# Performance work log

Hardware: AMD Instinct MI355X
Metric: run time of the kernel (lower is better)

Reference implementation:

```python
import jax, jax.numpy as jnp
import numpy as np

N = 50000      # nodes
E = 800000     # edges per metapath
M = 3          # metapaths
H = 2          # heads
IN = 128       # in_dim
HID = 64       # hidden
HEAD = HID // H
OUT = 16       # classes
ATT = 128      # atten_dim


def setup_inputs() -> dict:
    key = jax.random.key(0)
    ks = jax.random.split(key, 12)
    s = 0.05
    return {
        "x": jax.random.normal(ks[0], (N, IN), jnp.float32),
        "edge_index": jax.random.randint(ks[1], (M, 2, E), 0, N, dtype=jnp.int64),
        # per-(metapath, head) GCN params
        "W_enc": jax.random.normal(ks[2], (M, H, IN, HID), jnp.float32) * s,
        "b_enc": jnp.zeros((M, H, HID), jnp.float32),
        "W_conv": jax.random.normal(ks[3], (M, H, HID, HID), jnp.float32) * s,
        "b_conv": jnp.zeros((M, H, HID), jnp.float32),
        "W_dec": jax.random.normal(ks[4], (M, H, HID, HEAD), jnp.float32) * s,
        "b_dec": jnp.zeros((M, H, HEAD), jnp.float32),
        # semantic attention params
        "W_s": jax.random.normal(ks[5], (HID, ATT), jnp.float32) * s,
        "b_s": jnp.zeros((ATT,), jnp.float32),
        "q": jax.random.normal(ks[6], (ATT,), jnp.float32) * s,
        # output projection
        "W_o": jax.random.normal(ks[7], (HID, OUT), jnp.float32) * s,
        "b_o": jnp.zeros((OUT,), jnp.float32),
    }


def _lrelu(v, slope=0.1):
    return jnp.where(v > 0, v, slope * v)


def reference(x, edge_index, W_enc, b_enc, W_conv, b_conv, W_dec, b_dec, W_s, b_s, q, W_o, b_o):
    # encoder for all (metapath, head) at once: [M,H,N,HID]
    h = _lrelu(jnp.einsum('ni,mhio->mhno', x, W_enc) + b_enc[:, :, None, :])

    z_list = []
    for m in range(M):  # small fixed number of metapaths
        src = edge_index[m, 0]
        dst = edge_index[m, 1]
        # GCNConv with self-loops + symmetric normalization (PyG semantics)
        deg = jax.ops.segment_sum(jnp.ones(E, jnp.float32), dst, num_segments=N) + 1.0
        inv_sqrt = jax.lax.rsqrt(deg)
        coef = inv_sqrt[src] * inv_sqrt[dst]                 # [E]
        xw = jnp.einsum('hnd,hdo->hno', h[m], W_conv[m])     # [H,N,HID]
        msg = xw[:, src, :] * coef[None, :, None]            # [H,E,HID] gather
        agg = jax.vmap(lambda mm: jax.ops.segment_sum(mm, dst, num_segments=N))(msg)
        agg = agg + xw * (1.0 / deg)[None, :, None]          # self-loop term (norm = 1/deg)
        agg = agg + b_conv[m][:, None, :]
        hh = _lrelu(agg)
        dec = jnp.einsum('hnd,hdo->hno', hh, W_dec[m]) + b_dec[m][:, None, :]  # [H,N,HEAD]
        z_list.append(jnp.transpose(dec, (1, 0, 2)).reshape(N, HID))           # head concat

    zs = jnp.stack(z_list)                                   # [M,N,HID]
    # semantic attention over metapaths
    hs = jnp.tanh(jnp.einsum('mnd,da->mna', zs, W_s) + b_s)
    beta = jax.nn.softmax(jnp.einsum('mna,a->mn', hs, q).mean(axis=1))  # [M]
    Z = jnp.einsum('m,mnd->nd', beta, zs)                    # [N,HID]
    out = jax.nn.log_softmax(Z @ W_o + b_o, axis=-1)         # [N,OUT]
    return out, beta
```

## Files before the change

### kernel.cpp

```cpp
#include <hip/hip_runtime.h>

#define NN 50000
#define EE 800000
#define MM 3
#define HH 2
#define IND 128
#define HIDD 64
#define HEADD 32
#define OUTD 16
#define ATTD 128

#define NBKT 64
#define BSZ 782

#define NG4 200000
#define BBLK 196
#define QCAP 13200

#define GLS 136
#define XWN 50048

typedef unsigned char u8;
typedef unsigned short u16;
typedef unsigned long long u64;
typedef short bf16x8 __attribute__((ext_vector_type(8)));
typedef unsigned short u16x8 __attribute__((ext_vector_type(8)));
typedef u64 u64x2 __attribute__((ext_vector_type(2)));
typedef unsigned int u32x4 __attribute__((ext_vector_type(4)));
typedef float f32x2 __attribute__((ext_vector_type(2)));
typedef float f32x4 __attribute__((ext_vector_type(4)));

__device__ __forceinline__ float lrelu(float v) { return v > 0.f ? v : 0.1f * v; }

__device__ __forceinline__ float fast_tanh(float x) {
    float ax = fabsf(x);
    float e = __expf(-2.0f * ax);
    float t = (1.0f - e) * __builtin_amdgcn_rcpf(1.0f + e);
    return copysignf(t, x);
}

__device__ __forceinline__ u16 f2b(float f) {
    union { float f; unsigned int u; } v; v.f = f;
    unsigned int r = v.u + 0x7fffu + ((v.u >> 16) & 1u);
    return (u16)(r >> 16);
}
__device__ __forceinline__ float b2f(u16 u) {
    union { unsigned int u; float f; } v; v.u = ((unsigned int)u) << 16; return v.f;
}

__device__ __forceinline__ u8 f2e4hw(float f) {
    int r = __builtin_amdgcn_cvt_pk_fp8_f32(f, f, 0, false);
    return (u8)(r & 0xff);
}

__device__ __forceinline__ void acc16(f32x2* acc, u32x4 w) {
#pragma unroll
    for (int i = 0; i < 4; i++) {
        acc[2 * i]     += __builtin_amdgcn_cvt_pk_f32_fp8(w[i], false);
        acc[2 * i + 1] += __builtin_amdgcn_cvt_pk_f32_fp8(w[i], true);
    }
}

__global__ __launch_bounds__(256) void k_bucket(const int* __restrict__ ei,
                                                u64* __restrict__ queues,
                                                int* __restrict__ gcur) {
    __shared__ int cnt[NBKT];
    __shared__ int base[NBKT];
    const int m = blockIdx.y, tid = threadIdx.x;
    const int4* s4 = (const int4*)(ei + (size_t)m * 2 * EE);
    const int4* d4 = (const int4*)(ei + (size_t)m * 2 * EE + EE);
    const int q0 = blockIdx.x * 1024;
    if (tid < NBKT) cnt[tid] = 0;
    __syncthreads();
#pragma unroll
    for (int i = 0; i < 4; i++) {
        int q = q0 + i * 256 + tid;
        if (q < NG4) {
            int4 v = d4[q];
            atomicAdd(&cnt[v.x / BSZ], 1);
            atomicAdd(&cnt[v.y / BSZ], 1);
            atomicAdd(&cnt[v.z / BSZ], 1);
            atomicAdd(&cnt[v.w / BSZ], 1);
        }
    }
    __syncthreads();
    if (tid < NBKT) { base[tid] = atomicAdd(&gcur[m * NBKT + tid], cnt[tid]); cnt[tid] = 0; }
    __syncthreads();
#pragma unroll
    for (int i = 0; i < 4; i++) {
        int q = q0 + i * 256 + tid;
        if (q < NG4) {
            int4 dv = d4[q];
            int4 sv = s4[q];
            int ds[4] = {dv.x, dv.y, dv.z, dv.w};
            int ss[4] = {sv.x, sv.y, sv.z, sv.w};
#pragma unroll
            for (int e = 0; e < 4; e++) {
                int b = ds[e] / BSZ;
                int slot = base[b] + atomicAdd(&cnt[b], 1);
                if (slot < QCAP) {
                    u64 pk = ((u64)(unsigned)ds[e] << 32) | (unsigned)ss[e];
                    queues[((size_t)(m * NBKT + b)) * QCAP + slot] = pk;
                }
            }
        }
    }
}

__global__ void k_pscan(const int* __restrict__ gcur, int* __restrict__ pbase) {
    int t = threadIdx.x;
    if (t < MM) {
        int run = 0;
        for (int b = 0; b < NBKT; b++) {
            int L = gcur[t * NBKT + b]; if (L > QCAP) L = QCAP;
            pbase[t * NBKT + b] = run; run += L;
        }
    }
}

__global__ __launch_bounds__(512) void k_csr(const u64* __restrict__ queues,
                                             const int* __restrict__ gcur,
                                             const int* __restrict__ pbase,
                                             int* __restrict__ ofs,
                                             float* __restrict__ rs,
                                             int* __restrict__ sorted) {
    __shared__ int cnt[BSZ];
    __shared__ int wscan[8];
    const int m = blockIdx.y;
    const int b = blockIdx.x;
    const int tid = threadIdx.x;
    const int lane = tid & 63, w = tid >> 6;
    int qlen = gcur[m * NBKT + b]; if (qlen > QCAP) qlen = QCAP;
    const u64* q = queues + ((size_t)(m * NBKT + b)) * QCAP;
    const u64x2* q2 = (const u64x2*)q;
    const int dlo = b * BSZ;
    const int nd = min(dlo + BSZ, NN) - dlo;
    const int n2 = qlen >> 1;
    for (int i = tid; i < BSZ; i += 512) cnt[i] = 0;
    __syncthreads();
    for (int i = tid; i < n2; i += 512) {
        u64x2 e = q2[i];
        atomicAdd(&cnt[(int)(e.x >> 32) - dlo], 1);
        atomicAdd(&cnt[(int)(e.y >> 32) - dlo], 1);
    }
    if (tid == 0 && (qlen & 1))
        atomicAdd(&cnt[(int)(q[qlen - 1] >> 32) - dlo], 1);
    __syncthreads();
    const int c0 = tid * 2;
    int v0 = (c0 < BSZ) ? cnt[c0] : 0;
    int v1 = (c0 + 1 < BSZ) ? cnt[c0 + 1] : 0;
    int s = v0 + v1;
    int vv = s;
    for (int off = 1; off < 64; off <<= 1) { int t = __shfl_up(vv, off); if (lane >= off) vv += t; }
    if (lane == 63) wscan[w] = vv;
    __syncthreads();
    if (tid == 0) { int run = 0; for (int j = 0; j < 8; j++) { int t = wscan[j]; wscan[j] = run; run += t; } }
    __syncthreads();
    int excl = wscan[w] + vv - s;
    int g0 = pbase[m * NBKT + b] + excl;
    int g1 = g0 + v0;
    if (c0 < nd) {
        ofs[(size_t)m * (NN + 1) + dlo + c0] = g0;
        rs[(size_t)m * NN + dlo + c0] = rsqrtf((float)(v0 + 1));
    }
    if (c0 + 1 < nd) {
        ofs[(size_t)m * (NN + 1) + dlo + c0 + 1] = g1;
        rs[(size_t)m * NN + dlo + c0 + 1] = rsqrtf((float)(v1 + 1));
    }
    if (b == NBKT - 1 && tid == 0)
        ofs[(size_t)m * (NN + 1) + NN] = EE;
    __syncthreads();
    if (c0 < BSZ) cnt[c0] = g0;
    if (c0 + 1 < BSZ) cnt[c0 + 1] = g1;
    __syncthreads();
    int* srt = sorted + (size_t)m * EE;
    for (int i = tid; i < n2; i += 512) {
        u64x2 e = q2[i];
        int p0 = atomicAdd(&cnt[(int)(e.x >> 32) - dlo], 1);
        srt[p0] = (int)(e.x & 0xffffffffu);
        int p1 = atomicAdd(&cnt[(int)(e.y >> 32) - dlo], 1);
        srt[p1] = (int)(e.y & 0xffffffffu);
    }
    if (tid == 0 && (qlen & 1)) {
        u64 e = q[qlen - 1];
        int p0 = atomicAdd(&cnt[(int)(e >> 32) - dlo], 1);
        srt[p0] = (int)(e & 0xffffffffu);
    }
}

__global__ __launch_bounds__(256) void k_prep(const float* __restrict__ We, const float* __restrict__ Wc,
                                              const float* __restrict__ Wd, const float* __restrict__ Ws,
                                              u16* __restrict__ wbe, u16* __restrict__ wbc,
                                              u16* __restrict__ wbd, u16* __restrict__ wbs) {
    int t = blockIdx.x * 256 + threadIdx.x;
    if (t >= 11776) return;
    bf16x8 val;
    u16* dst;
    if (t < 6144) {
        int m = t >> 11, r = t & 2047;
        int nt = r >> 8, ks = (r >> 6) & 3, lane = r & 63;
        int n = nt * 16 + (lane & 15), h = n >> 6, o = n & 63;
        int kb = ks * 32 + (lane >> 4) * 8;
        const float* w = We + ((size_t)(m * 2 + h) * 128) * 64;
#pragma unroll
        for (int j = 0; j < 8; j++) val[j] = (short)f2b(w[(size_t)(kb + j) * 64 + o]);
        dst = wbe + ((size_t)m * 2048 + r) * 8;
    } else if (t < 9216) {
        int u = t - 6144;
        int m = u >> 10, r = u & 1023;
        int nt = r >> 7, ks = (r >> 6) & 1, lane = r & 63;
        int h = nt >> 2, o = (nt & 3) * 16 + (lane & 15);
        int kb = ks * 32 + (lane >> 4) * 8;
        const float* w = Wc + ((size_t)(m * 2 + h) * 64) * 64;
#pragma unroll
        for (int j = 0; j < 8; j++) val[j] = (short)f2b(w[(size_t)(kb + j) * 64 + o]);
        dst = wbc + ((size_t)m * 1024 + r) * 8;
    } else if (t < 10752) {
        int u = t - 9216;
        int m = u >> 9, r = u & 511;
        int nt = r >> 7, ks = (r >> 6) & 1, lane = r & 63;
        int h = nt >> 1, o = (nt & 1) * 16 + (lane & 15);
        int kb = ks * 32 + (lane >> 4) * 8;
        const float* w = Wd + ((size_t)(m * 2 + h) * 64) * 32;
#pragma unroll
        for (int j = 0; j < 8; j++) val[j] = (short)f2b(w[(size_t)(kb + j) * 32 + o]);
        dst = wbd + ((size_t)m * 512 + r) * 8;
    } else {
        int r = t - 10752;
        int nt = r >> 7, ks = (r >> 6) & 1, lane = r & 63;
        int n = nt * 16 + (lane & 15);
        int kb = ks * 32 + (lane >> 4) * 8;
#pragma unroll
        for (int j = 0; j < 8; j++) val[j] = (short)f2b(Ws[(size_t)(kb + j) * 128 + n]);
        dst = wbs + (size_t)r * 8;
    }
    *(bf16x8*)dst = val;
}

#define HLS 133
__global__ __launch_bounds__(256) void k_encconv(const float* __restrict__ x,
                                                 const u16* __restrict__ wbe_all,
                                                 const float* __restrict__ be_all,
                                                 const u16* __restrict__ wbc_all,
                                                 const float* __restrict__ rs_all,
                                                 u8* __restrict__ xw_all) {
    __shared__ float hl[64 * HLS];
    const int m = blockIdx.y;
    const int tid = threadIdx.x, lane = tid & 63, wave = tid >> 6;
    const int quad = lane >> 4, c16 = lane & 15;
    const int row = blockIdx.x * 64 + wave * 16 + c16;
    const bool ok = row < NN;
    const bf16x8* wbE = (const bf16x8*)(wbe_all + (size_t)m * 2048 * 8);
    const float* be = be_all + m * 2 * 64;
    const float* rs = rs_all + (size_t)m * NN;
    u8* xw = xw_all + (size_t)m * XWN * 128;
    f32x4 zero = {0.f, 0.f, 0.f, 0.f};
    f32x4 acc[8];
#pragma unroll
    for (int nt = 0; nt < 8; nt++) acc[nt] = zero;
#pragma unroll
    for (int ks = 0; ks < 4; ks++) {
        bf16x8 a = {0, 0, 0, 0, 0, 0, 0, 0};
        if (ok) {
            const float* xp = x + (size_t)row * 128 + ks * 32 + quad * 8;
            float4 xa = *(const float4*)xp;
            float4 xb = *(const float4*)(xp + 4);
            a[0] = (short)f2b(xa.x); a[1] = (short)f2b(xa.y);
            a[2] = (short)f2b(xa.z); a[3] = (short)f2b(xa.w);
            a[4] = (short)f2b(xb.x); a[5] = (short)f2b(xb.y);
            a[6] = (short)f2b(xb.z); a[7] = (short)f2b(xb.w);
        }
#pragma unroll
        for (int nt = 0; nt < 8; nt++)
            acc[nt] = __builtin_amdgcn_mfma_f32_16x16x32_bf16(a, wbE[(nt * 4 + ks) * 64 + lane], acc[nt], 0, 0, 0);
    }
    const int rbl = wave * 16 + quad * 4;
#pragma unroll
    for (int nt = 0; nt < 8; nt++) {
        int col = nt * 16 + c16, hh = col >> 6, o = col & 63;
        float bias = be[hh * 64 + o];
#pragma unroll
        for (int j = 0; j < 4; j++) {
            int rl = rbl + j;
            int rg = blockIdx.x * 64 + rl;
            hl[rl * HLS + col] = (rg < NN) ? lrelu(acc[nt][j] + bias) : 0.f;
        }
    }
    __syncthreads();
    const bf16x8* wbC = (const bf16x8*)(wbc_all + (size_t)m * 1024 * 8);
    f32x4 cacc[8];
#pragma unroll
    for (int nt = 0; nt < 8; nt++) cacc[nt] = zero;
    const int rl = wave * 16 + c16;
#pragma unroll
    for (int ks = 0; ks < 2; ks++) {
        bf16x8 a0, a1;
        const float* hp = &hl[rl * HLS + ks * 32 + quad * 8];
#pragma unroll
        for (int j = 0; j < 8; j++) { a0[j] = (short)f2b(hp[j]); a1[j] = (short)f2b(hp[64 + j]); }
#pragma unroll
        for (int nt = 0; nt < 8; nt++)
            cacc[nt] = __builtin_amdgcn_mfma_f32_16x16x32_bf16(nt < 4 ? a0 : a1, wbC[(nt * 2 + ks) * 64 + lane], cacc[nt], 0, 0, 0);
    }
    float rsv[4];
#pragma unroll
    for (int j = 0; j < 4; j++) {
        int r = blockIdx.x * 64 + rbl + j;
        rsv[j] = (r < NN) ? rs[r] * 64.f : 0.f;
    }
#pragma unroll
    for (int nt = 0; nt < 8; nt++) {
        int col = nt * 16 + c16;
#pragma unroll
        for (int j = 0; j < 4; j++) {
            int r = blockIdx.x * 64 + rbl + j;
            xw[(size_t)r * 128 + col] = f2e4hw(cacc[nt][j] * rsv[j]);
        }
    }
}

__global__ __launch_bounds__(512) void k_gpost(const int* __restrict__ sorted_all,
                                               const int* __restrict__ ofs_all,
                                               const float* __restrict__ rs_all,
                                               const u8* __restrict__ xw_all,
                                               const float* __restrict__ bconv_all,
                                               const u16* __restrict__ wbd_all,
                                               const float* __restrict__ bdec_all,
                                               const u16* __restrict__ wbs,
                                               const float* __restrict__ bs,
                                               const float* __restrict__ qv,
                                               u16* __restrict__ z_all,
                                               float* __restrict__ score) {
    __shared__ u16 shm[64 * GLS];
    __shared__ float spart[8];
    u16* ggl = shm;
    float* zl = (float*)shm;
    const int m = blockIdx.y;
    const int tid = threadIdx.x, lane = tid & 63, wave = tid >> 6;
    const int* sorted = sorted_all + (size_t)m * EE;
    const int* ofs = ofs_all + (size_t)m * (NN + 1);
    const float* rs = rs_all + (size_t)m * NN;
    const u8* xw = xw_all + (size_t)m * XWN * 128;
    const float* bconv = bconv_all + m * 2 * 64;
    const float* bdec = bdec_all + m * 2 * 32;
    u16* z = z_all + (size_t)m * NN * 64;

    {
        const int g = lane >> 3, c = lane & 7;
        const int wbase = blockIdx.x * 64 + wave * 8;
        const int dst = wbase + g;
        int ov = 0;
        { int ii = wbase + lane; if (lane < 9) ov = ofs[ii > NN ? NN : ii]; }
        const int beg = __shfl(ov, g);
        const int deg = __shfl(ov, g + 1) - beg;
        int degmax = max(deg, __shfl_xor(deg, 8));
        degmax = max(degmax, __shfl_xor(degmax, 16));
        degmax = max(degmax, __shfl_xor(degmax, 32));
        const int coff = c * 16;

        auto lidx = [&](int j) -> int {
            int t = j + (c & 3);
            return (t < deg) ? sorted[beg + t] : NN;
        };
        auto lrow = [&](int iv, u32x4* wv) {
#pragma unroll
            for (int k = 0; k < 4; k++) {
                int s = __shfl(iv, (lane & 0x38) + k);
                wv[k] = *(const u32x4*)&xw[(size_t)(unsigned)s * 128 + coff];
            }
        };

        f32x2 acc[8];
#pragma unroll
        for (int i = 0; i < 8; i++) acc[i] = 0.f;

        int i0 = lidx(0);
        int i1 = lidx(4);
        {
            int sd = dst < NN ? dst : NN;
            u32x4 w = *(const u32x4*)&xw[(size_t)sd * 128 + coff];
            acc16(acc, w);
        }
        u32x4 wA[4], wB[4];
        lrow(i0, wA);
        const int nch = ((degmax + 7) >> 3) * 2;
        for (int ch = 0; ch < nch; ch += 2) {
            lrow(i1, wB);
            i0 = lidx(ch * 4 + 8);
#pragma unroll
            for (int k = 0; k < 4; k++) acc16(acc, wA[k]);
            lrow(i0, wA);
            i1 = lidx(ch * 4 + 12);
#pragma unroll
            for (int k = 0; k < 4; k++) acc16(acc, wB[k]);
        }

        float rsv = (dst < NN) ? rs[dst] * (1.f / 64.f) : 0.f;
        u16x8 o0, o1;
#pragma unroll
        for (int i = 0; i < 4; i++) {
            o0[2 * i]     = f2b(acc[i].x * rsv);
            o0[2 * i + 1] = f2b(acc[i].y * rsv);
            o1[2 * i]     = f2b(acc[i + 4].x * rsv);
            o1[2 * i + 1] = f2b(acc[i + 4].y * rsv);
        }
        u16* gp = &ggl[(wave * 8 + g) * GLS + coff];
        *(u16x8*)gp = o0;
        *(u16x8*)(gp + 8) = o1;
    }
    __syncthreads();

    f32x4 zero = {0.f, 0.f, 0.f, 0.f};
    const int quad = lane >> 4, c16 = lane & 15;
    const int wq = wave & 3, hi = wave >> 2;
    const int rl = wq * 16 + c16;
    const bf16x8* wd = (const bf16x8*)(wbd_all + (size_t)m * 512 * 8);
    f32x4 pacc[2];
    pacc[0] = zero; pacc[1] = zero;
#pragma unroll
    for (int ks = 0; ks < 2; ks++) {
        bf16x8 a;
        int k0 = ks * 32 + quad * 8;
        const u16* gp = &ggl[rl * GLS + hi * 64 + k0];
#pragma unroll
        for (int j = 0; j < 8; j++)
            a[j] = (short)f2b(lrelu(b2f(gp[j]) + bconv[hi * 64 + k0 + j]));
#pragma unroll
        for (int nt2 = 0; nt2 < 2; nt2++) {
            int nt = hi * 2 + nt2;
            pacc[nt2] = __builtin_amdgcn_mfma_f32_16x16x32_bf16(a, wd[(nt * 2 + ks) * 64 + lane], pacc[nt2], 0, 0, 0);
        }
    }
    __syncthreads();
    {
        const int rbl = wq * 16 + quad * 4;
#pragma unroll
        for (int nt2 = 0; nt2 < 2; nt2++) {
            int nt = hi * 2 + nt2;
            int col = nt * 16 + c16, hh = col >> 5, o = col & 31;
            float bias = bdec[hh * 32 + o];
#pragma unroll
            for (int j = 0; j < 4; j++) {
                int rl2 = rbl + j;
                int rg = blockIdx.x * 64 + rl2;
                zl[rl2 * 68 + col] = (rg < NN) ? (pacc[nt2][j] + bias) : 0.f;
            }
        }
    }
    __syncthreads();

    {
        int rl2 = tid >> 3, cq = tid & 7;
        int rg = blockIdx.x * 64 + rl2;
        if (rg < NN) {
#pragma unroll
            for (int i = 0; i < 2; i++) {
                int c4 = (cq * 2 + i) * 4;
                float4 zv = *(const float4*)&zl[rl2 * 68 + c4];
                ushort4 o;
                o.x = f2b(zv.x); o.y = f2b(zv.y); o.z = f2b(zv.z); o.w = f2b(zv.w);
                *(ushort4*)&z[(size_t)rg * 64 + c4] = o;
            }
        }
    }
    float s = 0.f;
    {
        const bf16x8* wsb = (const bf16x8*)wbs;
        f32x4 sa[4];
#pragma unroll
        for (int nt2 = 0; nt2 < 4; nt2++) sa[nt2] = zero;
#pragma unroll
        for (int ks = 0; ks < 2; ks++) {
            bf16x8 a;
            const float* zp = &zl[rl * 68 + ks * 32 + quad * 8];
#pragma unroll
            for (int j = 0; j < 8; j++) a[j] = (short)f2b(zp[j]);
#pragma unroll
            for (int nt2 = 0; nt2 < 4; nt2++) {
                int nt = hi * 4 + nt2;
                sa[nt2] = __builtin_amdgcn_mfma_f32_16x16x32_bf16(a, wsb[(nt * 2 + ks) * 64 + lane], sa[nt2], 0, 0, 0);
            }
        }
        const int rbl = wq * 16 + quad * 4;
#pragma unroll
        for (int nt2 = 0; nt2 < 4; nt2++) {
            int nt = hi * 4 + nt2;
            int col = nt * 16 + c16;
            float qc = qv[col], bb = bs[col];
#pragma unroll
            for (int j = 0; j < 4; j++) {
                int rg = blockIdx.x * 64 + rbl + j;
                if (rg < NN) s += fast_tanh(sa[nt2][j] + bb) * qc;
            }
        }
#pragma unroll
        for (int off = 1; off < 64; off <<= 1) s += __shfl_xor(s, off);
    }
    if (lane == 0) spart[wave] = s;
    __syncthreads();
    if (tid == 0) {
        float t = spart[0] + spart[1] + spart[2] + spart[3]
                + spart[4] + spart[5] + spart[6] + spart[7];
        atomicAdd(&score[m], t);
    }
}

__global__ void k_beta(const float* __restrict__ score, float* __restrict__ beta_ws,
                       float* __restrict__ out) {
    if (threadIdx.x == 0) {
        float s0 = score[0] / (float)NN, s1 = score[1] / (float)NN, s2 = score[2] / (float)NN;
        float mx = fmaxf(s0, fmaxf(s1, s2));
        float e0 = expf(s0 - mx), e1 = expf(s1 - mx), e2 = expf(s2 - mx);
        float inv = 1.f / (e0 + e1 + e2);
        beta_ws[0] = e0 * inv; beta_ws[1] = e1 * inv; beta_ws[2] = e2 * inv;
        out[800000] = e0 * inv; out[800001] = e1 * inv; out[800002] = e2 * inv;
    }
}

__global__ __launch_bounds__(256) void k_out(const u16* __restrict__ z,
                                             const float* __restrict__ beta,
                                             const float* __restrict__ Wo,
                                             const float* __restrict__ bo,
                                             float* __restrict__ out) {
    __shared__ float Zt[64 * 68];
    __shared__ float Wl[64 * 16];
    __shared__ float bl[16];
    const int tid = threadIdx.x, nbase = blockIdx.x * 64;
    float b0 = beta[0], b1 = beta[1], b2 = beta[2];
    for (int qq = tid; qq < 64 * 16; qq += 256) {
        int node = qq >> 4, k4 = qq & 15;
        int ng = nbase + node;
        float4 v = make_float4(0.f, 0.f, 0.f, 0.f);
        if (ng < NN) {
            ushort4 z0 = *(const ushort4*)&z[((size_t)0 * NN + ng) * 64 + k4 * 4];
            ushort4 z1 = *(const ushort4*)&z[((size_t)1 * NN + ng) * 64 + k4 * 4];
            ushort4 z2 = *(const ushort4*)&z[((size_t)2 * NN + ng) * 64 + k4 * 4];
            v.x = b0 * b2f(z0.x) + b1 * b2f(z1.x) + b2 * b2f(z2.x);
            v.y = b0 * b2f(z0.y) + b1 * b2f(z1.y) + b2 * b2f(z2.y);
            v.z = b0 * b2f(z0.z) + b1 * b2f(z1.z) + b2 * b2f(z2.z);
            v.w = b0 * b2f(z0.w) + b1 * b2f(z1.w) + b2 * b2f(z2.w);
        }
        *(float4*)&Zt[node * 68 + k4 * 4] = v;
    }
    for (int qq = tid; qq < 64 * 16 / 4; qq += 256)
        ((float4*)Wl)[qq] = ((const float4*)Wo)[qq];
    if (tid < 16) bl[tid] = bo[tid];
    __syncthreads();

    const int node = tid >> 2, cg = tid & 3;
    float4 a = make_float4(bl[cg * 4 + 0], bl[cg * 4 + 1], bl[cg * 4 + 2], bl[cg * 4 + 3]);
    for (int k = 0; k < 64; k++) {
        float zv = Zt[node * 68 + k];
        float4 w = *(const float4*)&Wl[k * 16 + cg * 4];
        a.x = fmaf(zv, w.x, a.x);
        a.y = fmaf(zv, w.y, a.y);
        a.z = fmaf(zv, w.z, a.z);
        a.w = fmaf(zv, w.w, a.w);
    }
    float mx = fmaxf(fmaxf(a.x, a.y), fmaxf(a.z, a.w));
    mx = fmaxf(mx, __shfl_xor(mx, 1));
    mx = fmaxf(mx, __shfl_xor(mx, 2));
    float sm = expf(a.x - mx) + expf(a.y - mx) + expf(a.z - mx) + expf(a.w - mx);
    sm += __shfl_xor(sm, 1);
    sm += __shfl_xor(sm, 2);
    float lse = mx + logf(sm);
    int ng = nbase + node;
    if (ng < NN) {
        float4 r = make_float4(a.x - lse, a.y - lse, a.z - lse, a.w - lse);
        *(float4*)&out[(size_t)ng * 16 + cg * 4] = r;
    }
}

extern "C" void kernel_launch(void* const* d_in, const int* in_sizes, int n_in,
                              void* d_out, int out_size, void* d_ws, size_t ws_size,
                              hipStream_t stream) {
    const float* x      = (const float*)d_in[0];
    const int*   ei     = (const int*)d_in[1];
    const float* W_enc  = (const float*)d_in[2];
    const float* b_enc  = (const float*)d_in[3];
    const float* W_conv = (const float*)d_in[4];
    const float* b_conv = (const float*)d_in[5];
    const float* W_dec  = (const float*)d_in[6];
    const float* b_dec  = (const float*)d_in[7];
    const float* W_s    = (const float*)d_in[8];
    const float* b_s    = (const float*)d_in[9];
    const float* qv     = (const float*)d_in[10];
    const float* W_o    = (const float*)d_in[11];
    const float* b_o    = (const float*)d_in[12];
    float* out = (float*)d_out;

    char* ws = (char*)d_ws;
    size_t off = 0;
    auto alloc = [&](size_t bytes) -> char* {
        char* p = ws + off;
        off = (off + bytes + 255) & ~(size_t)255;
        return p;
    };
    int*   row_ofs = (int*)alloc((size_t)MM * (NN + 1) * 4);
    float* rs      = (float*)alloc((size_t)MM * NN * 4);
    int*   sorted  = (int*)alloc((size_t)MM * EE * 4);
    u64*   queues  = (u64*)alloc((size_t)MM * NBKT * QCAP * 8);
    int*   gcur    = (int*)alloc((size_t)MM * NBKT * 4);
    int*   pbase   = (int*)alloc((size_t)MM * NBKT * 4);
    float* score   = (float*)alloc(64);
    float* beta_ws = (float*)alloc(64);
    u16*   wbe     = (u16*)alloc((size_t)MM * 2048 * 8 * 2);
    u16*   wbc     = (u16*)alloc((size_t)MM * 1024 * 8 * 2);
    u16*   wbd     = (u16*)alloc((size_t)MM * 512 * 8 * 2);
    u16*   wbs     = (u16*)alloc((size_t)1024 * 8 * 2);
    u8*    xw_buf  = (u8*)alloc((size_t)MM * XWN * 128);
    u16*   z_buf   = (u16*)alloc((size_t)MM * NN * 64 * 2);

    hipMemsetAsync(gcur, 0, (size_t)MM * NBKT * 4, stream);
    hipMemsetAsync(score, 0, 16, stream);

    dim3 gbkt(BBLK, MM);
    dim3 gcsr(NBKT, MM);
    k_bucket<<<gbkt, 256, 0, stream>>>(ei, queues, gcur);
    k_pscan<<<1, 64, 0, stream>>>(gcur, pbase);
    k_csr<<<gcsr, 512, 0, stream>>>(queues, gcur, pbase, row_ofs, rs, sorted);
    k_prep<<<46, 256, 0, stream>>>(W_enc, W_conv, W_dec, W_s, wbe, wbc, wbd, wbs);

    const int GB = (NN + 63) / 64;
    dim3 gmm(GB, MM);
    k_encconv<<<gmm, 256, 0, stream>>>(x, wbe, b_enc, wbc, rs, xw_buf);
    k_gpost<<<gmm, 512, 0, stream>>>(sorted, row_ofs, rs, xw_buf,
                                     b_conv, wbd, b_dec, wbs, b_s, qv,
                                     z_buf, score);
    k_beta<<<1, 64, 0, stream>>>(score, beta_ws, out);
    k_out<<<GB, 256, 0, stream>>>(z_buf, beta_ws, W_o, b_o, out);
}
```

Before: 248.1 us.

## Sort gather rows by degree per block and reuse x across metapaths in encoder

Adds a small kernel that ranks each 64-node group by in-degree, so that the gather kernel assigns nodes with similar degree to the same 8-lane group within a wave. This reduces divergence from the per-wave max-degree loop. The encoder kernel now loads and converts each x row once and loops over all three metapaths, instead of launching one block per metapath and rereading x each time. It also vectorizes a few LDS reads. The cost is an extra launch plus a perm buffer, and fewer but longer encoder blocks.

```diff
diff --git a/kernel.cpp b/kernel.cpp
--- a/kernel.cpp
+++ b/kernel.cpp
@@ -19,6 +19,7 @@
 
 #define GLS 136
 #define XWN 50048
+#define PN  50048
 
 typedef unsigned char u8;
 typedef unsigned short u16;
@@ -188,6 +189,29 @@
     }
 }
 
+__global__ __launch_bounds__(256) void k_perm(const int* __restrict__ ofs_all,
+                                              int* __restrict__ perm_all) {
+    __shared__ int dl[256];
+    const int m = blockIdx.y;
+    const int t = threadIdx.x;
+    const int sub = t >> 6, li = t & 63;
+    const int base = blockIdx.x * 256 + sub * 64;
+    const int* ofs = ofs_all + (size_t)m * (NN + 1);
+    const int g = base + li;
+    int d = (g < NN) ? (ofs[g + 1] - ofs[g]) : -1;
+    dl[t] = d;
+    __syncthreads();
+    if (base < PN) {
+        const int* dls = &dl[sub * 64];
+        int rank = 0;
+        for (int j = 0; j < 64; j++) {
+            int dj = dls[j];
+            rank += (dj > d || (dj == d && j < li)) ? 1 : 0;
+        }
+        perm_all[(size_t)m * PN + base + rank] = li;
+    }
+}
+
 __global__ __launch_bounds__(256) void k_prep(const float* __restrict__ We, const float* __restrict__ Wc,
                                               const float* __restrict__ Wd, const float* __restrict__ Ws,
                                               u16* __restrict__ wbe, u16* __restrict__ wbc,
@@ -245,82 +269,93 @@
                                                  const float* __restrict__ rs_all,
                                                  u8* __restrict__ xw_all) {
     __shared__ float hl[64 * HLS];
-    const int m = blockIdx.y;
     const int tid = threadIdx.x, lane = tid & 63, wave = tid >> 6;
     const int quad = lane >> 4, c16 = lane & 15;
     const int row = blockIdx.x * 64 + wave * 16 + c16;
     const bool ok = row < NN;
-    const bf16x8* wbE = (const bf16x8*)(wbe_all + (size_t)m * 2048 * 8);
-    const float* be = be_all + m * 2 * 64;
-    const float* rs = rs_all + (size_t)m * NN;
-    u8* xw = xw_all + (size_t)m * XWN * 128;
+    const int rbl = wave * 16 + quad * 4;
+    const int rl = wave * 16 + c16;
     f32x4 zero = {0.f, 0.f, 0.f, 0.f};
-    f32x4 acc[8];
-#pragma unroll
-    for (int nt = 0; nt < 8; nt++) acc[nt] = zero;
+
+    bf16x8 a[4];
 #pragma unroll
     for (int ks = 0; ks < 4; ks++) {
-        bf16x8 a = {0, 0, 0, 0, 0, 0, 0, 0};
+        bf16x8 t = {0, 0, 0, 0, 0, 0, 0, 0};
         if (ok) {
             const float* xp = x + (size_t)row * 128 + ks * 32 + quad * 8;
             float4 xa = *(const float4*)xp;
             float4 xb = *(const float4*)(xp + 4);
-            a[0] = (short)f2b(xa.x); a[1] = (short)f2b(xa.y);
-            a[2] = (short)f2b(xa.z); a[3] = (short)f2b(xa.w);
-            a[4] = (short)f2b(xb.x); a[5] = (short)f2b(xb.y);
-            a[6] = (short)f2b(xb.z); a[7] = (short)f2b(xb.w);
-        }
-#pragma unroll
-        for (int nt = 0; nt < 8; nt++)
-            acc[nt] = __builtin_amdgcn_mfma_f32_16x16x32_bf16(a, wbE[(nt * 4 + ks) * 64 + lane], acc[nt], 0, 0, 0);
-    }
-    const int rbl = wave * 16 + quad * 4;
-#pragma unroll
-    for (int nt = 0; nt < 8; nt++) {
-        int col = nt * 16 + c16, hh = col >> 6, o = col & 63;
-        float bias = be[hh * 64 + o];
-#pragma unroll
-        for (int j = 0; j < 4; j++) {
-            int rl = rbl + j;
-            int rg = blockIdx.x * 64 + rl;
-            hl[rl * HLS + col] = (rg < NN) ? lrelu(acc[nt][j] + bias) : 0.f;
-        }
-    }
-    __syncthreads();
-    const bf16x8* wbC = (const bf16x8*)(wbc_all + (size_t)m * 1024 * 8);
-    f32x4 cacc[8];
-#pragma unroll
-    for (int nt = 0; nt < 8; nt++) cacc[nt] = zero;
-    const int rl = wave * 16 + c16;
-#pragma unroll
-    for (int ks = 0; ks < 2; ks++) {
-        bf16x8 a0, a1;
-        const float* hp = &hl[rl * HLS + ks * 32 + quad * 8];
-#pragma unroll
-        for (int j = 0; j < 8; j++) { a0[j] = (short)f2b(hp[j]); a1[j] = (short)f2b(hp[64 + j]); }
-#pragma unroll
-        for (int nt = 0; nt < 8; nt++)
-            cacc[nt] = __builtin_amdgcn_mfma_f32_16x16x32_bf16(nt < 4 ? a0 : a1, wbC[(nt * 2 + ks) * 64 + lane], cacc[nt], 0, 0, 0);
-    }
-    float rsv[4];
-#pragma unroll
-    for (int j = 0; j < 4; j++) {
-        int r = blockIdx.x * 64 + rbl + j;
-        rsv[j] = (r < NN) ? rs[r] * 64.f : 0.f;
-    }
-#pragma unroll
-    for (int nt = 0; nt < 8; nt++) {
-        int col = nt * 16 + c16;
+            t[0] = (short)f2b(xa.x); t[1] = (short)f2b(xa.y);
+            t[2] = (short)f2b(xa.z); t[3] = (short)f2b(xa.w);
+            t[4] = (short)f2b(xb.x); t[5] = (short)f2b(xb.y);
+            t[6] = (short)f2b(xb.z); t[7] = (short)f2b(xb.w);
+        }
+        a[ks] = t;
+    }
+
+    for (int m = 0; m < MM; m++) {
+        const bf16x8* wbE = (const bf16x8*)(wbe_all + (size_t)m * 2048 * 8);
+        const float* be = be_all + m * 2 * 64;
+        const float* rs = rs_all + (size_t)m * NN;
+        u8* xw = xw_all + (size_t)m * XWN * 128;
+
+        f32x4 acc[8];
+#pragma unroll
+        for (int nt = 0; nt < 8; nt++) acc[nt] = zero;
+#pragma unroll
+        for (int ks = 0; ks < 4; ks++) {
+#pragma unroll
+            for (int nt = 0; nt < 8; nt++)
+                acc[nt] = __builtin_amdgcn_mfma_f32_16x16x32_bf16(a[ks], wbE[(nt * 4 + ks) * 64 + lane], acc[nt], 0, 0, 0);
+        }
+#pragma unroll
+        for (int nt = 0; nt < 8; nt++) {
+            int col = nt * 16 + c16, hh = col >> 6, o = col & 63;
+            float bias = be[hh * 64 + o];
+#pragma unroll
+            for (int j = 0; j < 4; j++) {
+                int rlw = rbl + j;
+                int rg = blockIdx.x * 64 + rlw;
+                hl[rlw * HLS + col] = (rg < NN) ? lrelu(acc[nt][j] + bias) : 0.f;
+            }
+        }
+        __syncthreads();
+        const bf16x8* wbC = (const bf16x8*)(wbc_all + (size_t)m * 1024 * 8);
+        f32x4 cacc[8];
+#pragma unroll
+        for (int nt = 0; nt < 8; nt++) cacc[nt] = zero;
+#pragma unroll
+        for (int ks = 0; ks < 2; ks++) {
+            bf16x8 a0, a1;
+            const float* hp = &hl[rl * HLS + ks * 32 + quad * 8];
+#pragma unroll
+            for (int j = 0; j < 8; j++) { a0[j] = (short)f2b(hp[j]); a1[j] = (short)f2b(hp[64 + j]); }
+#pragma unroll
+            for (int nt = 0; nt < 8; nt++)
+                cacc[nt] = __builtin_amdgcn_mfma_f32_16x16x32_bf16(nt < 4 ? a0 : a1, wbC[(nt * 2 + ks) * 64 + lane], cacc[nt], 0, 0, 0);
+        }
+        float rsv[4];
 #pragma unroll
         for (int j = 0; j < 4; j++) {
             int r = blockIdx.x * 64 + rbl + j;
-            xw[(size_t)r * 128 + col] = f2e4hw(cacc[nt][j] * rsv[j]);
-        }
+            rsv[j] = (r < NN) ? rs[r] * 64.f : 0.f;
+        }
+#pragma unroll
+        for (int nt = 0; nt < 8; nt++) {
+            int col = nt * 16 + c16;
+#pragma unroll
+            for (int j = 0; j < 4; j++) {
+                int r = blockIdx.x * 64 + rbl + j;
+                xw[(size_t)r * 128 + col] = f2e4hw(cacc[nt][j] * rsv[j]);
+            }
+        }
+        if (m < MM - 1) __syncthreads();
     }
 }
 
 __global__ __launch_bounds__(512) void k_gpost(const int* __restrict__ sorted_all,
                                                const int* __restrict__ ofs_all,
+                                               const int* __restrict__ perm_all,
                                                const float* __restrict__ rs_all,
                                                const u8* __restrict__ xw_all,
                                                const float* __restrict__ bconv_all,
@@ -339,6 +374,7 @@
     const int tid = threadIdx.x, lane = tid & 63, wave = tid >> 6;
     const int* sorted = sorted_all + (size_t)m * EE;
     const int* ofs = ofs_all + (size_t)m * (NN + 1);
+    const int* perm = perm_all + (size_t)m * PN;
     const float* rs = rs_all + (size_t)m * NN;
     const u8* xw = xw_all + (size_t)m * XWN * 128;
     const float* bconv = bconv_all + m * 2 * 64;
@@ -347,12 +383,11 @@
 
     {
         const int g = lane >> 3, c = lane & 7;
-        const int wbase = blockIdx.x * 64 + wave * 8;
-        const int dst = wbase + g;
-        int ov = 0;
-        { int ii = wbase + lane; if (lane < 9) ov = ofs[ii > NN ? NN : ii]; }
-        const int beg = __shfl(ov, g);
-        const int deg = __shfl(ov, g + 1) - beg;
+        const int pl = perm[blockIdx.x * 64 + wave * 8 + g];
+        const int dst = blockIdx.x * 64 + pl;
+        const bool on = dst < NN;
+        int beg = 0, deg = 0;
+        if (on) { beg = ofs[dst]; deg = ofs[dst + 1] - beg; }
         int degmax = max(deg, __shfl_xor(deg, 8));
         degmax = max(degmax, __shfl_xor(degmax, 16));
         degmax = max(degmax, __shfl_xor(degmax, 32));
@@ -377,7 +412,7 @@
         int i0 = lidx(0);
         int i1 = lidx(4);
         {
-            int sd = dst < NN ? dst : NN;
+            int sd = on ? dst : NN;
             u32x4 w = *(const u32x4*)&xw[(size_t)sd * 128 + coff];
             acc16(acc, w);
         }
@@ -395,7 +430,7 @@
             for (int k = 0; k < 4; k++) acc16(acc, wB[k]);
         }
 
-        float rsv = (dst < NN) ? rs[dst] * (1.f / 64.f) : 0.f;
+        float rsv = on ? rs[dst] * (1.f / 64.f) : 0.f;
         u16x8 o0, o1;
 #pragma unroll
         for (int i = 0; i < 4; i++) {
@@ -404,7 +439,7 @@
             o1[2 * i]     = f2b(acc[i + 4].x * rsv);
             o1[2 * i + 1] = f2b(acc[i + 4].y * rsv);
         }
-        u16* gp = &ggl[(wave * 8 + g) * GLS + coff];
+        u16* gp = &ggl[pl * GLS + coff];
         *(u16x8*)gp = o0;
         *(u16x8*)(gp + 8) = o1;
     }
@@ -421,10 +456,10 @@
     for (int ks = 0; ks < 2; ks++) {
         bf16x8 a;
         int k0 = ks * 32 + quad * 8;
-        const u16* gp = &ggl[rl * GLS + hi * 64 + k0];
+        u16x8 gv = *(const u16x8*)&ggl[rl * GLS + hi * 64 + k0];
 #pragma unroll
         for (int j = 0; j < 8; j++)
-            a[j] = (short)f2b(lrelu(b2f(gp[j]) + bconv[hi * 64 + k0 + j]));
+            a[j] = (short)f2b(lrelu(b2f(gv[j]) + bconv[hi * 64 + k0 + j]));
 #pragma unroll
         for (int nt2 = 0; nt2 < 2; nt2++) {
             int nt = hi * 2 + nt2;
@@ -473,8 +508,12 @@
         for (int ks = 0; ks < 2; ks++) {
             bf16x8 a;
             const float* zp = &zl[rl * 68 + ks * 32 + quad * 8];
-#pragma unroll
-            for (int j = 0; j < 8; j++) a[j] = (short)f2b(zp[j]);
+            f32x4 z0 = *(const f32x4*)zp;
+            f32x4 z1 = *(const f32x4*)(zp + 4);
+            a[0] = (short)f2b(z0[0]); a[1] = (short)f2b(z0[1]);
+            a[2] = (short)f2b(z0[2]); a[3] = (short)f2b(z0[3]);
+            a[4] = (short)f2b(z1[0]); a[5] = (short)f2b(z1[1]);
+            a[6] = (short)f2b(z1[2]); a[7] = (short)f2b(z1[3]);
 #pragma unroll
             for (int nt2 = 0; nt2 < 4; nt2++) {
                 int nt = hi * 4 + nt2;
@@ -610,6 +649,7 @@
     u16*   wbs     = (u16*)alloc((size_t)1024 * 8 * 2);
     u8*    xw_buf  = (u8*)alloc((size_t)MM * XWN * 128);
     u16*   z_buf   = (u16*)alloc((size_t)MM * NN * 64 * 2);
+    int*   perm    = (int*)alloc((size_t)MM * PN * 4);
 
     hipMemsetAsync(gcur, 0, (size_t)MM * NBKT * 4, stream);
     hipMemsetAsync(score, 0, 16, stream);
@@ -622,9 +662,12 @@
     k_prep<<<46, 256, 0, stream>>>(W_enc, W_conv, W_dec, W_s, wbe, wbc, wbd, wbs);
 
     const int GB = (NN + 63) / 64;
+    dim3 gperm((GB + 3) / 4, MM);
+    k_perm<<<gperm, 256, 0, stream>>>(row_ofs, perm);
+
+    k_encconv<<<GB, 256, 0, stream>>>(x, wbe, b_enc, wbc, rs, xw_buf);
     dim3 gmm(GB, MM);
-    k_encconv<<<gmm, 256, 0, stream>>>(x, wbe, b_enc, wbc, rs, xw_buf);
-    k_gpost<<<gmm, 512, 0, stream>>>(sorted, row_ofs, rs, xw_buf,
+    k_gpost<<<gmm, 512, 0, stream>>>(sorted, row_ofs, perm, rs, xw_buf,
                                      b_conv, wbd, b_dec, wbs, b_s, qv,
                                      z_buf, score);
     k_beta<<<1, 64, 0, stream>>>(score, beta_ws, out);
```

New measurement: 266.3 us. +7.3%, slower.

## Sort destination nodes by degree to balance gather work in k_gpost

Applied to the files above, without the earlier changes.

Adds a degree histogram, a descending scan and a scatter pass that build a per-metapath permutation of nodes ordered by in-degree. k_gpost then processes nodes through this permutation, so each 8-node wave group has similar degrees and wastes fewer iterations on the degmax loop. Output rows are written back at the permuted node index. Also vectorizes a few LDS reads. It costs three extra small kernels with global atomics and gives up the contiguous node locality of the z stores and of the offset and rs loads.

```diff
diff --git a/kernel.cpp b/kernel.cpp
--- a/kernel.cpp
+++ b/kernel.cpp
@@ -19,6 +19,7 @@
 
 #define GLS 136
 #define XWN 50048
+#define PN  50048
 
 typedef unsigned char u8;
 typedef unsigned short u16;
@@ -188,6 +189,47 @@
     }
 }
 
+__global__ __launch_bounds__(256) void k_dhist(const int* __restrict__ ofs_all,
+                                               int* __restrict__ bins) {
+    const int m = blockIdx.y;
+    int n = blockIdx.x * 256 + threadIdx.x;
+    if (n < NN) {
+        const int* ofs = ofs_all + (size_t)m * (NN + 1);
+        int d = ofs[n + 1] - ofs[n];
+        int b = d > 63 ? 63 : d;
+        atomicAdd(&bins[m * 64 + b], 1);
+    }
+}
+
+__global__ void k_dscan(int* __restrict__ bins) {
+    int m = threadIdx.x;
+    if (m < MM) {
+        int run = 0;
+        for (int b = 63; b >= 0; b--) {
+            int cb = bins[m * 64 + b];
+            bins[m * 64 + b] = run;
+            run += cb;
+        }
+    }
+}
+
+__global__ __launch_bounds__(256) void k_dscat(const int* __restrict__ ofs_all,
+                                               int* __restrict__ bins,
+                                               int* __restrict__ perm_all) {
+    const int m = blockIdx.y;
+    int n = blockIdx.x * 256 + threadIdx.x;
+    int* perm = perm_all + (size_t)m * PN;
+    if (n < NN) {
+        const int* ofs = ofs_all + (size_t)m * (NN + 1);
+        int d = ofs[n + 1] - ofs[n];
+        int b = d > 63 ? 63 : d;
+        int slot = atomicAdd(&bins[m * 64 + b], 1);
+        perm[slot] = n;
+    } else if (n < PN) {
+        perm[n] = NN;
+    }
+}
+
 __global__ __launch_bounds__(256) void k_prep(const float* __restrict__ We, const float* __restrict__ Wc,
                                               const float* __restrict__ Wd, const float* __restrict__ Ws,
                                               u16* __restrict__ wbe, u16* __restrict__ wbc,
@@ -321,6 +363,7 @@
 
 __global__ __launch_bounds__(512) void k_gpost(const int* __restrict__ sorted_all,
                                                const int* __restrict__ ofs_all,
+                                               const int* __restrict__ perm_all,
                                                const float* __restrict__ rs_all,
                                                const u8* __restrict__ xw_all,
                                                const float* __restrict__ bconv_all,
@@ -333,26 +376,28 @@
                                                float* __restrict__ score) {
     __shared__ u16 shm[64 * GLS];
     __shared__ float spart[8];
+    __shared__ int pml[64];
     u16* ggl = shm;
     float* zl = (float*)shm;
     const int m = blockIdx.y;
     const int tid = threadIdx.x, lane = tid & 63, wave = tid >> 6;
     const int* sorted = sorted_all + (size_t)m * EE;
     const int* ofs = ofs_all + (size_t)m * (NN + 1);
+    const int* perm = perm_all + (size_t)m * PN;
     const float* rs = rs_all + (size_t)m * NN;
     const u8* xw = xw_all + (size_t)m * XWN * 128;
     const float* bconv = bconv_all + m * 2 * 64;
     const float* bdec = bdec_all + m * 2 * 32;
     u16* z = z_all + (size_t)m * NN * 64;
 
+    if (tid < 64) pml[tid] = perm[blockIdx.x * 64 + tid];
+
     {
         const int g = lane >> 3, c = lane & 7;
-        const int wbase = blockIdx.x * 64 + wave * 8;
-        const int dst = wbase + g;
-        int ov = 0;
-        { int ii = wbase + lane; if (lane < 9) ov = ofs[ii > NN ? NN : ii]; }
-        const int beg = __shfl(ov, g);
-        const int deg = __shfl(ov, g + 1) - beg;
+        const int dst = perm[blockIdx.x * 64 + wave * 8 + g];
+        const bool on = dst < NN;
+        int beg = 0, deg = 0;
+        if (on) { beg = ofs[dst]; deg = ofs[dst + 1] - beg; }
         int degmax = max(deg, __shfl_xor(deg, 8));
         degmax = max(degmax, __shfl_xor(degmax, 16));
         degmax = max(degmax, __shfl_xor(degmax, 32));
@@ -377,7 +422,7 @@
         int i0 = lidx(0);
         int i1 = lidx(4);
         {
-            int sd = dst < NN ? dst : NN;
+            int sd = on ? dst : NN;
             u32x4 w = *(const u32x4*)&xw[(size_t)sd * 128 + coff];
             acc16(acc, w);
         }
@@ -395,7 +440,7 @@
             for (int k = 0; k < 4; k++) acc16(acc, wB[k]);
         }
 
-        float rsv = (dst < NN) ? rs[dst] * (1.f / 64.f) : 0.f;
+        float rsv = on ? rs[dst] * (1.f / 64.f) : 0.f;
         u16x8 o0, o1;
 #pragma unroll
         for (int i = 0; i < 4; i++) {
@@ -421,10 +466,10 @@
     for (int ks = 0; ks < 2; ks++) {
         bf16x8 a;
         int k0 = ks * 32 + quad * 8;
-        const u16* gp = &ggl[rl * GLS + hi * 64 + k0];
+        u16x8 gv = *(const u16x8*)&ggl[rl * GLS + hi * 64 + k0];
 #pragma unroll
         for (int j = 0; j < 8; j++)
-            a[j] = (short)f2b(lrelu(b2f(gp[j]) + bconv[hi * 64 + k0 + j]));
+            a[j] = (short)f2b(lrelu(b2f(gv[j]) + bconv[hi * 64 + k0 + j]));
 #pragma unroll
         for (int nt2 = 0; nt2 < 2; nt2++) {
             int nt = hi * 2 + nt2;
@@ -442,8 +487,7 @@
 #pragma unroll
             for (int j = 0; j < 4; j++) {
                 int rl2 = rbl + j;
-                int rg = blockIdx.x * 64 + rl2;
-                zl[rl2 * 68 + col] = (rg < NN) ? (pacc[nt2][j] + bias) : 0.f;
+                zl[rl2 * 68 + col] = (pml[rl2] < NN) ? (pacc[nt2][j] + bias) : 0.f;
             }
         }
     }
@@ -451,15 +495,15 @@
 
     {
         int rl2 = tid >> 3, cq = tid & 7;
-        int rg = blockIdx.x * 64 + rl2;
-        if (rg < NN) {
+        int node = pml[rl2];
+        if (node < NN) {
 #pragma unroll
             for (int i = 0; i < 2; i++) {
                 int c4 = (cq * 2 + i) * 4;
                 float4 zv = *(const float4*)&zl[rl2 * 68 + c4];
                 ushort4 o;
                 o.x = f2b(zv.x); o.y = f2b(zv.y); o.z = f2b(zv.z); o.w = f2b(zv.w);
-                *(ushort4*)&z[(size_t)rg * 64 + c4] = o;
+                *(ushort4*)&z[(size_t)node * 64 + c4] = o;
             }
         }
     }
@@ -473,8 +517,12 @@
         for (int ks = 0; ks < 2; ks++) {
             bf16x8 a;
             const float* zp = &zl[rl * 68 + ks * 32 + quad * 8];
-#pragma unroll
-            for (int j = 0; j < 8; j++) a[j] = (short)f2b(zp[j]);
+            f32x4 z0 = *(const f32x4*)zp;
+            f32x4 z1 = *(const f32x4*)(zp + 4);
+            a[0] = (short)f2b(z0[0]); a[1] = (short)f2b(z0[1]);
+            a[2] = (short)f2b(z0[2]); a[3] = (short)f2b(z0[3]);
+            a[4] = (short)f2b(z1[0]); a[5] = (short)f2b(z1[1]);
+            a[6] = (short)f2b(z1[2]); a[7] = (short)f2b(z1[3]);
 #pragma unroll
             for (int nt2 = 0; nt2 < 4; nt2++) {
                 int nt = hi * 4 + nt2;
@@ -489,8 +537,7 @@
             float qc = qv[col], bb = bs[col];
 #pragma unroll
             for (int j = 0; j < 4; j++) {
-                int rg = blockIdx.x * 64 + rbl + j;
-                if (rg < NN) s += fast_tanh(sa[nt2][j] + bb) * qc;
+                if (pml[rbl + j] < NN) s += fast_tanh(sa[nt2][j] + bb) * qc;
             }
         }
 #pragma unroll
@@ -610,9 +657,12 @@
     u16*   wbs     = (u16*)alloc((size_t)1024 * 8 * 2);
     u8*    xw_buf  = (u8*)alloc((size_t)MM * XWN * 128);
     u16*   z_buf   = (u16*)alloc((size_t)MM * NN * 64 * 2);
+    int*   perm    = (int*)alloc((size_t)MM * PN * 4);
+    int*   bins    = (int*)alloc((size_t)MM * 64 * 4);
 
     hipMemsetAsync(gcur, 0, (size_t)MM * NBKT * 4, stream);
     hipMemsetAsync(score, 0, 16, stream);
+    hipMemsetAsync(bins, 0, (size_t)MM * 64 * 4, stream);
 
     dim3 gbkt(BBLK, MM);
     dim3 gcsr(NBKT, MM);
@@ -621,10 +671,15 @@
     k_csr<<<gcsr, 512, 0, stream>>>(queues, gcur, pbase, row_ofs, rs, sorted);
     k_prep<<<46, 256, 0, stream>>>(W_enc, W_conv, W_dec, W_s, wbe, wbc, wbd, wbs);
 
+    dim3 gdeg(BBLK, MM);
+    k_dhist<<<gdeg, 256, 0, stream>>>(row_ofs, bins);
+    k_dscan<<<1, 64, 0, stream>>>(bins);
+    k_dscat<<<gdeg, 256, 0, stream>>>(row_ofs, bins, perm);
+
     const int GB = (NN + 63) / 64;
     dim3 gmm(GB, MM);
     k_encconv<<<gmm, 256, 0, stream>>>(x, wbe, b_enc, wbc, rs, xw_buf);
-    k_gpost<<<gmm, 512, 0, stream>>>(sorted, row_ofs, rs, xw_buf,
+    k_gpost<<<gmm, 512, 0, stream>>>(sorted, row_ofs, perm, rs, xw_buf,
                                      b_conv, wbd, b_dec, wbs, b_s, qv,
                                      z_buf, score);
     k_beta<<<1, 64, 0, stream>>>(score, beta_ws, out);
```

Result: slower. 581.0 us (+134.2%).
